# Kernel optimization log

Hardware: AMD Instinct MI355X
Metric: run time of the kernel (lower is better)

## Reference

```python
import jax, jax.numpy as jnp
from jax import lax
import numpy as np

NUM_HEADS = 16
NUM_HEADS_KV = 4
HEAD_DIM = 128
D_CONV = 4
ROT_DIM = 128
ROT_BASE = 10000.0
CAUSAL = True


def setup_inputs() -> dict:
    key = jax.random.key(0)
    ks = jax.random.split(key, 7)
    B, S, E = 2, 2048, 2048
    QKV = HEAD_DIM * (NUM_HEADS + 2 * NUM_HEADS_KV)  # 3072
    return {
        "x": jax.random.normal(ks[0], (B, S, E), jnp.float32),
        "W_in": jax.random.normal(ks[1], (QKV, E), jnp.float32) * 0.02,
        "b_in": jax.random.normal(ks[2], (QKV,), jnp.float32) * 0.02,
        "conv_w": jax.random.normal(ks[3], (QKV, D_CONV), jnp.float32) * 0.1,
        "conv_b": jax.random.normal(ks[4], (QKV,), jnp.float32) * 0.02,
        "W_out": jax.random.normal(ks[5], (E, NUM_HEADS * HEAD_DIM), jnp.float32) * 0.02,
        "b_out": jax.random.normal(ks[6], (E,), jnp.float32) * 0.02,
    }


def _rotary(x, cos, sin):
    # x: [B,S,H,D], non-interleaved rotary over first ROT_DIM dims (here full D)
    x1, x2 = x[..., : ROT_DIM // 2], x[..., ROT_DIM // 2 : ROT_DIM]
    c = cos[None, :, None, :]
    s = sin[None, :, None, :]
    rot = jnp.concatenate([x1 * c - x2 * s, x2 * c + x1 * s], axis=-1)
    return jnp.concatenate([rot, x[..., ROT_DIM:]], axis=-1)


def reference(x, W_in, b_in, conv_w, conv_b, W_out, b_out):
    B, S, E = x.shape
    QKV = conv_w.shape[0]
    # fused in-projection
    qkv = jnp.einsum("bse,fe->bsf", x, W_in) + b_in  # [B,S,QKV]
    # depthwise causal conv1d (left pad d_conv-1, equivalent to torch pad+trim)
    qkv_t = jnp.transpose(qkv, (0, 2, 1))  # [B,C,S]
    qkv_t = jnp.pad(qkv_t, ((0, 0), (0, 0), (D_CONV - 1, 0)))
    conv = lax.conv_general_dilated(
        qkv_t, conv_w[:, None, :], window_strides=(1,), padding="VALID",
        feature_group_count=QKV, dimension_numbers=("NCH", "OIH", "NCH"))
    qkv = jnp.transpose(conv + conv_b[None, :, None], (0, 2, 1))  # [B,S,QKV]
    # split q / kv
    q_dim = NUM_HEADS * HEAD_DIM
    q = qkv[..., :q_dim].reshape(B, S, NUM_HEADS, HEAD_DIM)
    kv = qkv[..., q_dim:].reshape(B, S, 2, NUM_HEADS_KV, HEAD_DIM)
    k, v = kv[:, :, 0], kv[:, :, 1]
    # rotary embedding on q and k
    t = jnp.arange(S, dtype=jnp.float32)
    inv_freq = 1.0 / (ROT_BASE ** (jnp.arange(0, ROT_DIM, 2, dtype=jnp.float32) / ROT_DIM))
    freqs = t[:, None] * inv_freq[None, :]  # [S, ROT_DIM/2]
    cos, sin = jnp.cos(freqs), jnp.sin(freqs)
    q = _rotary(q, cos, sin)
    k = _rotary(k, cos, sin)
    # GQA: repeat kv heads
    rep = NUM_HEADS // NUM_HEADS_KV
    k = jnp.repeat(k, rep, axis=2)  # [B,S,H,D]
    v = jnp.repeat(v, rep, axis=2)
    scale = 1.0 / jnp.sqrt(jnp.float32(HEAD_DIM))
    scores = jnp.einsum("bshd,bthd->bhst", q, k) * scale  # [B,H,S,S]
    if CAUSAL:
        mask = jnp.tril(jnp.ones((S, S), dtype=bool))
        scores = jnp.where(mask[None, None], scores, jnp.finfo(scores.dtype).min)
    attn = jax.nn.softmax(scores, axis=-1)
    ctx = jnp.einsum("bhst,bthd->bshd", attn, v).reshape(B, S, q_dim)
    return jnp.einsum("bsf,ef->bse", ctx, W_out) + b_out
```

## Files before the change

kernel.cpp:

```cpp
#include <hip/hip_runtime.h>
#include <hip/hip_bf16.h>

#define B_   2
#define S_   2048
#define E_   2048
#define QKV_ 3072
#define NH   16
#define NKV  4
#define HD   128
#define SL   16

typedef __attribute__((ext_vector_type(8))) short bf16x8;
typedef __attribute__((ext_vector_type(4))) float f32x4;
typedef unsigned short u16;
typedef unsigned int   u32;

__device__ __forceinline__ float bf2f(u16 u) {
  union { u32 i; float f; } v; v.i = ((u32)u) << 16; return v.f;
}
__device__ __forceinline__ u16 f2bf(float f) {
  union { float f; u32 u; } v; v.f = f;
  return (u16)((v.u + 0x7FFFu + ((v.u >> 16) & 1u)) >> 16);
}
__device__ __forceinline__ u32 pkbf(float a, float b) {
  __hip_bfloat162 h = __float22bfloat162_rn(float2{a, b});
  u32 r; __builtin_memcpy(&r, &h, 4); return r;
}
__device__ __forceinline__ float ex2(float x) { return __builtin_amdgcn_exp2f(x); }
__device__ __forceinline__ void load_lds16(const u16* g, u16* l) {
  __builtin_amdgcn_global_load_lds((const __attribute__((address_space(1))) void*)g,
                                   (__attribute__((address_space(3))) void*)l, 16, 0, 0);
}

__global__ __launch_bounds__(256) void f2b_conv(const float* __restrict__ in,
                                                u16* __restrict__ out, int n4) {
  const int i = blockIdx.x * 256 + threadIdx.x;
  if (i >= n4) return;
  const float4 v = ((const float4*)in)[i];
  ushort4 o;
  o.x = f2bf(v.x); o.y = f2bf(v.y); o.z = f2bf(v.z); o.w = f2bf(v.w);
  ((ushort4*)out)[i] = o;
}

__global__ __launch_bounds__(256) void rope_tab(float* __restrict__ c,
                                                float* __restrict__ s) {
  const int idx = blockIdx.x * 256 + threadIdx.x;
  const int t = idx >> 6, i = idx & 63;
  const float invf = powf(10000.0f, -(float)i * (1.0f / 64.0f));
  float sn, cs;
  sincosf((float)t * invf, &sn, &cs);
  c[idx] = cs; s[idx] = sn;
}

template <int OUT_BF16>
__global__ __launch_bounds__(512, 2) void gemm256(const u16* __restrict__ A,
                                                  const u16* __restrict__ Bm,
                                                  const float* __restrict__ bias,
                                                  void* __restrict__ C,
                                                  int M, int N, int K) {
  __shared__ u16 sm[2][2][256 * 64];
  const int tid = threadIdx.x;
  const int lane = tid & 63;
  const int wave = tid >> 6;
  const int wm = wave >> 2, wn = wave & 3;
  const int L15 = lane & 15, Lq = lane >> 4;
  const int m0 = blockIdx.y * 256, n0 = blockIdx.x * 256;
  const int NT = K >> 6;

  const int srow = tid >> 3;
  const int sdst = (tid & 7) * 8;
  const int ssrc = ((tid & 7) ^ (srow & 7)) * 8;

  auto stageA = [&](int T, int h, int j) {
    const int row = h * 128 + j * 64 + srow;
    load_lds16(A + (size_t)(m0 + row) * K + T * 64 + ssrc,
               &sm[T & 1][0][row * 64 + sdst]);
  };
  auto stageB = [&](int T, int h, int j) {
    const int row = h * 128 + j * 64 + srow;
    load_lds16(Bm + (size_t)(n0 + row) * K + T * 64 + ssrc,
               &sm[T & 1][1][row * 64 + sdst]);
  };
  auto rdA = [&](int p, int ms, int mf, int kk) -> bf16x8 {
    const int row = wm * 128 + ms * 64 + mf * 16 + L15;
    const int u = (kk * 4 + Lq) ^ (row & 7);
    return *(const bf16x8*)&sm[p][0][row * 64 + u * 8];
  };
  auto rdB = [&](int p, int ns, int nf, int kk) -> bf16x8 {
    const int row = wn * 64 + ns * 32 + nf * 16 + L15;
    const int u = (kk * 4 + Lq) ^ (row & 7);
    return *(const bf16x8*)&sm[p][1][row * 64 + u * 8];
  };

  f32x4 acc[8][4] = {};

  stageA(0, 0, 0); stageA(0, 0, 1);
  stageB(0, 0, 0); stageB(0, 0, 1);
  stageA(0, 1, 0); stageA(0, 1, 1);
  stageB(0, 1, 0); stageB(0, 1, 1);
  stageB(1, 0, 0); stageB(1, 0, 1);
  stageA(1, 0, 0); stageA(1, 0, 1);
  asm volatile("s_waitcnt vmcnt(4)" ::: "memory");
  __builtin_amdgcn_s_barrier();

  bf16x8 af[4][2], bf0[2][2], bf1[2][2];

#define MFMA_QUAD(MS, NS, BF)                                                     \
  __builtin_amdgcn_s_setprio(1);                                                  \
  _Pragma("unroll")                                                               \
  for (int kk = 0; kk < 2; ++kk)                                                  \
    _Pragma("unroll")                                                             \
    for (int mf = 0; mf < 4; ++mf)                                                \
      _Pragma("unroll")                                                           \
      for (int nf = 0; nf < 2; ++nf)                                              \
        acc[MS * 4 + mf][NS * 2 + nf] = __builtin_amdgcn_mfma_f32_16x16x32_bf16(  \
            af[mf][kk], BF[nf][kk], acc[MS * 4 + mf][NS * 2 + nf], 0, 0, 0);      \
  __builtin_amdgcn_s_setprio(0);

  for (int T = 0; T < NT; ++T) {
    const int p = T & 1;
#pragma unroll
    for (int mf = 0; mf < 4; ++mf)
#pragma unroll
      for (int kk = 0; kk < 2; ++kk) af[mf][kk] = rdA(p, 0, mf, kk);
#pragma unroll
    for (int nf = 0; nf < 2; ++nf)
#pragma unroll
      for (int kk = 0; kk < 2; ++kk) bf0[nf][kk] = rdB(p, 0, nf, kk);
    if (T + 1 < NT) { stageA(T + 1, 1, 0); stageA(T + 1, 1, 1); }
    __builtin_amdgcn_s_barrier();
    MFMA_QUAD(0, 0, bf0)
    __builtin_amdgcn_s_barrier();
#pragma unroll
    for (int nf = 0; nf < 2; ++nf)
#pragma unroll
      for (int kk = 0; kk < 2; ++kk) bf1[nf][kk] = rdB(p, 1, nf, kk);
    if (T + 1 < NT) { stageB(T + 1, 1, 0); stageB(T + 1, 1, 1); }
    __builtin_amdgcn_s_barrier();
    MFMA_QUAD(0, 1, bf1)
    __builtin_amdgcn_s_barrier();
#pragma unroll
    for (int mf = 0; mf < 4; ++mf)
#pragma unroll
      for (int kk = 0; kk < 2; ++kk) af[mf][kk] = rdA(p, 1, mf, kk);
    if (T + 2 < NT) { stageB(T + 2, 0, 0); stageB(T + 2, 0, 1); }
    __builtin_amdgcn_s_barrier();
    MFMA_QUAD(1, 0, bf0)
    __builtin_amdgcn_s_barrier();
    if (T + 2 < NT) {
      stageA(T + 2, 0, 0); stageA(T + 2, 0, 1);
      asm volatile("s_waitcnt vmcnt(4)" ::: "memory");
    } else {
      asm volatile("s_waitcnt vmcnt(0)" ::: "memory");
    }
    __builtin_amdgcn_s_barrier();
    MFMA_QUAD(1, 1, bf1)
    __builtin_amdgcn_s_barrier();
  }
#undef MFMA_QUAD

#pragma unroll
  for (int ms = 0; ms < 2; ++ms)
#pragma unroll
    for (int mf = 0; mf < 4; ++mf) {
      const int grow0 = m0 + wm * 128 + ms * 64 + mf * 16 + Lq * 4;
#pragma unroll
      for (int ns = 0; ns < 2; ++ns)
#pragma unroll
        for (int nf = 0; nf < 2; ++nf) {
          const int gcol = n0 + wn * 64 + ns * 32 + nf * 16 + L15;
          const float bv = bias[gcol];
          const f32x4 v = acc[ms * 4 + mf][ns * 2 + nf];
#pragma unroll
          for (int r = 0; r < 4; ++r) {
            const float o = v[r] + bv;
            if (OUT_BF16) ((u16*)C)[(size_t)(grow0 + r) * N + gcol] = f2bf(o);
            else          ((float*)C)[(size_t)(grow0 + r) * N + gcol] = o;
          }
        }
    }
}

__global__ __launch_bounds__(512, 2) void gemm_n128(const u16* __restrict__ A,
                                                    const u16* __restrict__ Bm,
                                                    const float* __restrict__ bias,
                                                    float* __restrict__ C,
                                                    int M, int N, int K) {
  __shared__ u16 sm[2][24576];
  const int tid = threadIdx.x, lane = tid & 63, wave = tid >> 6;
  const int wm = wave >> 1, wn = wave & 1;
  const int L15 = lane & 15, Lq = lane >> 4;
  const int m0 = blockIdx.y * 256, n0 = blockIdx.x * 128;
  const int NT = K >> 6;

  const int srow = tid >> 3;
  const int sdst = (tid & 7) * 8;
  const int ssrc = ((tid & 7) ^ (srow & 7)) * 8;

  auto stage6 = [&](int T) {
#pragma unroll
    for (int c = 0; c < 4; ++c) {
      const int row = c * 64 + srow;
      load_lds16(A + (size_t)(m0 + row) * K + T * 64 + ssrc,
                 &sm[T & 1][row * 64 + sdst]);
    }
#pragma unroll
    for (int c = 0; c < 2; ++c) {
      const int row = c * 64 + srow;
      load_lds16(Bm + (size_t)(n0 + row) * K + T * 64 + ssrc,
                 &sm[T & 1][16384 + row * 64 + sdst]);
    }
  };

  f32x4 acc[4][4] = {};
  stage6(0);

  for (int T = 0; T < NT; ++T) {
    const int p = T & 1;
    if (T + 1 < NT) {
      stage6(T + 1);
      asm volatile("s_waitcnt vmcnt(6)" ::: "memory");
    } else {
      asm volatile("s_waitcnt vmcnt(0)" ::: "memory");
    }
    __builtin_amdgcn_s_barrier();
    bf16x8 af[4][2], bfr[4][2];
#pragma unroll
    for (int mf = 0; mf < 4; ++mf)
#pragma unroll
      for (int kk = 0; kk < 2; ++kk) {
        const int row = wm * 64 + mf * 16 + L15;
        const int u = (kk * 4 + Lq) ^ (row & 7);
        af[mf][kk] = *(const bf16x8*)&sm[p][row * 64 + u * 8];
      }
#pragma unroll
    for (int nf = 0; nf < 4; ++nf)
#pragma unroll
      for (int kk = 0; kk < 2; ++kk) {
        const int row = wn * 64 + nf * 16 + L15;
        const int u = (kk * 4 + Lq) ^ (row & 7);
        bfr[nf][kk] = *(const bf16x8*)&sm[p][16384 + row * 64 + u * 8];
      }
    __builtin_amdgcn_s_setprio(1);
#pragma unroll
    for (int kk = 0; kk < 2; ++kk)
#pragma unroll
      for (int mf = 0; mf < 4; ++mf)
#pragma unroll
        for (int nf = 0; nf < 4; ++nf)
          acc[mf][nf] = __builtin_amdgcn_mfma_f32_16x16x32_bf16(
              af[mf][kk], bfr[nf][kk], acc[mf][nf], 0, 0, 0);
    __builtin_amdgcn_s_setprio(0);
    __builtin_amdgcn_s_barrier();
  }

#pragma unroll
  for (int mf = 0; mf < 4; ++mf) {
    const int grow0 = m0 + wm * 64 + mf * 16 + Lq * 4;
#pragma unroll
    for (int nf = 0; nf < 4; ++nf) {
      const int gcol = n0 + wn * 64 + nf * 16 + L15;
      const float bv = bias[gcol];
#pragma unroll
      for (int r = 0; r < 4; ++r)
        C[(size_t)(grow0 + r) * N + gcol] = acc[mf][nf][r] + bv;
    }
  }
}

__global__ __launch_bounds__(256) void conv_rope(const u16* __restrict__ qkv,
                                                 const float* __restrict__ cw,
                                                 const float* __restrict__ cb,
                                                 const float* __restrict__ ct,
                                                 const float* __restrict__ st,
                                                 u16* __restrict__ qo,
                                                 u16* __restrict__ ko,
                                                 u16* __restrict__ vtmp) {
  const int blk = blockIdx.x;
  const int b = blk >> 7;
  const int s0 = (blk & 127) * SL;
  const u16* qb = qkv + (size_t)b * S_ * QKV_;

  for (int u = threadIdx.x; u < 896; u += 256) {
    if (u < 640) {
      const int hs = u >> 5, ip = u & 31, i = ip * 2;
      int f1; u16* outbase; float scale;
      if (hs < 16) {
        f1 = hs * HD + i;
        outbase = qo + (size_t)(b * NH + hs) * S_ * HD;
        scale = 0.08838834764831845f * 1.4426950408889634f;
      } else {
        f1 = NH * HD + (hs - 16) * HD + i;
        outbase = ko + (size_t)(b * NKV + (hs - 16)) * S_ * HD;
        scale = 1.0f;
      }
      const int f2 = f1 + 64;
      const float4 wA0 = *(const float4*)&cw[f1 * 4];
      const float4 wA1 = *(const float4*)&cw[(f1 + 1) * 4];
      const float4 wB0 = *(const float4*)&cw[f2 * 4];
      const float4 wB1 = *(const float4*)&cw[(f2 + 1) * 4];
      const float cA0 = cb[f1], cA1 = cb[f1 + 1], cB0 = cb[f2], cB1 = cb[f2 + 1];
      float A0[3], A1[3], B0[3], B1[3];
#pragma unroll
      for (int j = 0; j < 3; ++j) {
        const int t = s0 - 3 + j;
        if (t >= 0) {
          const u32 pa = *(const u32*)&qb[(size_t)t * QKV_ + f1];
          const u32 pb = *(const u32*)&qb[(size_t)t * QKV_ + f2];
          A0[j] = bf2f((u16)pa); A1[j] = bf2f((u16)(pa >> 16));
          B0[j] = bf2f((u16)pb); B1[j] = bf2f((u16)(pb >> 16));
        } else { A0[j] = A1[j] = B0[j] = B1[j] = 0.f; }
      }
      for (int s = s0; s < s0 + SL; ++s) {
        const u32 pa = *(const u32*)&qb[(size_t)s * QKV_ + f1];
        const u32 pb = *(const u32*)&qb[(size_t)s * QKV_ + f2];
        const float nA0 = bf2f((u16)pa), nA1 = bf2f((u16)(pa >> 16));
        const float nB0 = bf2f((u16)pb), nB1 = bf2f((u16)(pb >> 16));
        const float x1a = cA0 + wA0.x * A0[0] + wA0.y * A0[1] + wA0.z * A0[2] + wA0.w * nA0;
        const float x1b = cA1 + wA1.x * A1[0] + wA1.y * A1[1] + wA1.z * A1[2] + wA1.w * nA1;
        const float x2a = cB0 + wB0.x * B0[0] + wB0.y * B0[1] + wB0.z * B0[2] + wB0.w * nB0;
        const float x2b = cB1 + wB1.x * B1[0] + wB1.y * B1[1] + wB1.z * B1[2] + wB1.w * nB1;
        const float2 cs = *(const float2*)&ct[s * 64 + i];
        const float2 sn = *(const float2*)&st[s * 64 + i];
        u16* outp = outbase + (size_t)s * HD;
        *(u32*)&outp[i]      = pkbf((x1a * cs.x - x2a * sn.x) * scale,
                                    (x1b * cs.y - x2b * sn.y) * scale);
        *(u32*)&outp[i + 64] = pkbf((x2a * cs.x + x1a * sn.x) * scale,
                                    (x2b * cs.y + x1b * sn.y) * scale);
        A0[0] = A0[1]; A0[1] = A0[2]; A0[2] = nA0;
        A1[0] = A1[1]; A1[1] = A1[2]; A1[2] = nA1;
        B0[0] = B0[1]; B0[1] = B0[2]; B0[2] = nB0;
        B1[0] = B1[1]; B1[1] = B1[2]; B1[2] = nB1;
      }
    } else {
      const int vu = u - 640, h = vu >> 6, d = (vu & 63) * 2;
      const int f = (NH + NKV) * HD + h * HD + d;
      const float4 w0 = *(const float4*)&cw[f * 4];
      const float4 w1 = *(const float4*)&cw[(f + 1) * 4];
      const float c0 = cb[f], c1 = cb[f + 1];
      float V0[3], V1[3];
#pragma unroll
      for (int j = 0; j < 3; ++j) {
        const int t = s0 - 3 + j;
        if (t >= 0) {
          const u32 p = *(const u32*)&qb[(size_t)t * QKV_ + f];
          V0[j] = bf2f((u16)p); V1[j] = bf2f((u16)(p >> 16));
        } else { V0[j] = V1[j] = 0.f; }
      }
      u16* vrow = vtmp + (size_t)(b * NKV + h) * S_ * HD + d;
      for (int s = s0; s < s0 + SL; ++s) {
        const u32 p = *(const u32*)&qb[(size_t)s * QKV_ + f];
        const float n0 = bf2f((u16)p), n1 = bf2f((u16)(p >> 16));
        const float v0 = c0 + w0.x * V0[0] + w0.y * V0[1] + w0.z * V0[2] + w0.w * n0;
        const float v1 = c1 + w1.x * V1[0] + w1.y * V1[1] + w1.z * V1[2] + w1.w * n1;
        *(u32*)&vrow[(size_t)s * HD] = pkbf(v0, v1);
        V0[0] = V0[1]; V0[1] = V0[2]; V0[2] = n0;
        V1[0] = V1[1]; V1[1] = V1[2]; V1[2] = n1;
      }
    }
  }
}

__global__ __launch_bounds__(256) void vtrans(const u16* __restrict__ vin,
                                              u16* __restrict__ vout) {
  __shared__ u16 t[64][72];
  const int bh = blockIdx.z;
  const int d0 = blockIdx.y * 64;
  const int s0 = blockIdx.x * 64;
  const u16* ip = vin + ((size_t)bh * S_ + s0) * HD + d0;
  const int r = threadIdx.x >> 4, c4 = (threadIdx.x & 15) * 4;
#pragma unroll
  for (int j = 0; j < 4; ++j) {
    const ushort4 v = *(const ushort4*)&ip[(size_t)(r + j * 16) * HD + c4];
    t[c4 + 0][r + j * 16] = v.x;
    t[c4 + 1][r + j * 16] = v.y;
    t[c4 + 2][r + j * 16] = v.z;
    t[c4 + 3][r + j * 16] = v.w;
  }
  __syncthreads();
  const int dl = threadIdx.x >> 2, sc = (threadIdx.x & 3) * 16;
  u16* op = vout + (size_t)bh * HD * S_ + (size_t)(d0 + dl) * S_ + s0 + sc;
  *(bf16x8*)op       = *(const bf16x8*)&t[dl][sc];
  *(bf16x8*)(op + 8) = *(const bf16x8*)&t[dl][sc + 8];
}

__global__ __launch_bounds__(256, 2) void attn(const u16* __restrict__ q,
                                               const u16* __restrict__ k,
                                               const u16* __restrict__ v,
                                               u16* __restrict__ ctx) {
  __shared__ u16 Ks[2][64 * 128];
  __shared__ u16 Vs[128 * 64];
  __shared__ u16 P[4][16 * 64];
  const int tid = threadIdx.x, wave = tid >> 6, lane = tid & 63;
  const int L15 = lane & 15, Lq = lane >> 4;
  const int bh = blockIdx.y;
  const int b = bh >> 4, h = bh & 15, hk = h >> 2;

  const u16* kb = k + (size_t)(b * NKV + hk) * S_ * HD;
  const u16* vb = v + (size_t)(b * NKV + hk) * HD * S_;

  const int rx = L15 & 7;
  int koff[4], voff[2], poff[2];
#pragma unroll
  for (int c = 0; c < 4; ++c) koff[c] = ((c * 4 + Lq) ^ rx) * 8;
#pragma unroll
  for (int kc = 0; kc < 2; ++kc) {
    voff[kc] = ((kc * 4 + Lq) ^ rx) * 8;
    poff[kc] = L15 * 64 + ((kc * 4 + Lq) ^ rx) * 8;
  }

  const int ksl = tid >> 4, kcp = tid & 15;
  const int vsl = tid >> 3, vcp = tid & 7;

  for (int pass = 0; pass < 2; ++pass) {
    const int qt = pass ? (31 - blockIdx.x) : blockIdx.x;
    const int q0 = qt * 64;
    const int base = q0 + wave * 16;

    bf16x8 qf[4];
    {
      const u16* qp = q + ((size_t)bh * S_ + base + L15) * HD + Lq * 8;
#pragma unroll
      for (int c = 0; c < 4; ++c) qf[c] = *(const bf16x8*)(qp + c * 32);
    }

    f32x4 acc[8] = {};
    float m_i[4], l_i[4];
#pragma unroll
    for (int r = 0; r < 4; ++r) { m_i[r] = -1e30f; l_i[r] = 0.f; }

    const int ktmax = qt + 1;

#pragma unroll
    for (int j = 0; j < 4; ++j) {
      const int krow = j * 16 + ksl;
      load_lds16(kb + (size_t)krow * HD + (kcp ^ (krow & 7)) * 8,
                 &Ks[0][(krow * 16 + kcp) * 8]);
      const int vrow = j * 32 + vsl;
      load_lds16(vb + (size_t)vrow * S_ + (vcp ^ (vrow & 7)) * 8,
                 &Vs[(vrow * 8 + vcp) * 8]);
    }
    __syncthreads();

    for (int kt = 0; kt < ktmax; ++kt) {
      const int k0 = kt * 64;
      const int cur = kt & 1;
      if (kt > 0) {
#pragma unroll
        for (int j = 0; j < 4; ++j) {
          const int vrow = j * 32 + vsl;
          load_lds16(vb + (size_t)vrow * S_ + k0 + (vcp ^ (vrow & 7)) * 8,
                     &Vs[(vrow * 8 + vcp) * 8]);
        }
      }
      if (kt + 1 < ktmax) {
        const int kn = k0 + 64;
#pragma unroll
        for (int j = 0; j < 4; ++j) {
          const int krow = j * 16 + ksl;
          load_lds16(kb + (size_t)(kn + krow) * HD + (kcp ^ (krow & 7)) * 8,
                     &Ks[cur ^ 1][(krow * 16 + kcp) * 8]);
        }
      }
      f32x4 sc[4];
#pragma unroll
      for (int nt = 0; nt < 4; ++nt) sc[nt] = f32x4{0.f, 0.f, 0.f, 0.f};
#pragma unroll
      for (int nt = 0; nt < 4; ++nt) {
#pragma unroll
        for (int c = 0; c < 4; ++c) {
          const bf16x8 kf = *(const bf16x8*)&Ks[cur][(nt * 16 + L15) * 128 + koff[c]];
          sc[nt] = __builtin_amdgcn_mfma_f32_16x16x32_bf16(qf[c], kf, sc[nt], 0, 0, 0);
        }
      }
      if (k0 + 63 > base) {
#pragma unroll
        for (int nt = 0; nt < 4; ++nt) {
          const int col = k0 + nt * 16 + L15;
#pragma unroll
          for (int r = 0; r < 4; ++r) {
            const int row = base + Lq * 4 + r;
            if (col > row) sc[nt][r] = -1e30f;
          }
        }
      }
      float mloc[4];
      bool nm = false;
#pragma unroll
      for (int r = 0; r < 4; ++r) {
        float m = fmaxf(fmaxf(sc[0][r], sc[1][r]), fmaxf(sc[2][r], sc[3][r]));
        m = fmaxf(m, __shfl_xor(m, 1));
        m = fmaxf(m, __shfl_xor(m, 2));
        m = fmaxf(m, __shfl_xor(m, 4));
        m = fmaxf(m, __shfl_xor(m, 8));
        mloc[r] = m;
        nm |= (m > m_i[r]);
      }
      const bool anynew = (__ballot(nm) != 0ull);
      float rsum[4];
      {
        float mnew[4];
#pragma unroll
        for (int r = 0; r < 4; ++r) {
          mnew[r] = anynew ? fmaxf(m_i[r], mloc[r]) : m_i[r];
          rsum[r] = 0.f;
        }
        float pv[4][4];
#pragma unroll
        for (int nt = 0; nt < 4; ++nt)
#pragma unroll
          for (int r = 0; r < 4; ++r) {
            pv[nt][r] = ex2(sc[nt][r] - mnew[r]);
            rsum[r] += pv[nt][r];
          }
#pragma unroll
        for (int nt = 0; nt < 4; ++nt) {
          const int cch = nt * 2 + (L15 >> 3), clo = L15 & 7;
#pragma unroll
          for (int rp = 0; rp < 2; ++rp) {
            const u32 pk = pkbf(pv[nt][rp * 2], pv[nt][rp * 2 + 1]);
            const int row0 = Lq * 4 + rp * 2;
            P[wave][row0 * 64 + (((cch ^ (row0 & 7)) << 3) | clo)] = (u16)pk;
            const int row1 = row0 + 1;
            P[wave][row1 * 64 + (((cch ^ (row1 & 7)) << 3) | clo)] = (u16)(pk >> 16);
          }
        }
        if (anynew) {
          float alpha[4];
#pragma unroll
          for (int r = 0; r < 4; ++r) {
            alpha[r] = ex2(m_i[r] - mnew[r]);
            m_i[r] = mnew[r];
          }
#pragma unroll
          for (int dt = 0; dt < 8; ++dt)
#pragma unroll
            for (int r = 0; r < 4; ++r) acc[dt][r] *= alpha[r];
#pragma unroll
          for (int r = 0; r < 4; ++r) l_i[r] *= alpha[r];
        }
      }
#pragma unroll
      for (int r = 0; r < 4; ++r) {
        float s = rsum[r];
        s += __shfl_xor(s, 1);
        s += __shfl_xor(s, 2);
        s += __shfl_xor(s, 4);
        s += __shfl_xor(s, 8);
        l_i[r] += s;
      }
      __syncthreads();
      {
        bf16x8 pa[2];
#pragma unroll
        for (int kc = 0; kc < 2; ++kc)
          pa[kc] = *(const bf16x8*)&P[wave][poff[kc]];
#pragma unroll
        for (int dt = 0; dt < 8; ++dt)
#pragma unroll
          for (int kc = 0; kc < 2; ++kc) {
            const bf16x8 vf = *(const bf16x8*)&Vs[(dt * 16 + L15) * 64 + voff[kc]];
            acc[dt] = __builtin_amdgcn_mfma_f32_16x16x32_bf16(pa[kc], vf, acc[dt], 0, 0, 0);
          }
      }
      __syncthreads();
    }
    {
      float inv[4];
#pragma unroll
      for (int r = 0; r < 4; ++r) inv[r] = 1.f / l_i[r];
      u16* cp = ctx + ((size_t)b * S_ + base) * (NH * HD) + h * HD;
#pragma unroll
      for (int dt = 0; dt < 8; ++dt)
#pragma unroll
        for (int rp = 0; rp < 2; ++rp) {
          const u32 pk = pkbf(acc[dt][rp * 2] * inv[rp * 2],
                              acc[dt][rp * 2 + 1] * inv[rp * 2 + 1]);
          cp[(size_t)(Lq * 4 + rp * 2) * (NH * HD) + dt * 16 + L15] = (u16)pk;
          cp[(size_t)(Lq * 4 + rp * 2 + 1) * (NH * HD) + dt * 16 + L15] = (u16)(pk >> 16);
        }
    }
  }
}

extern "C" void kernel_launch(void* const* d_in, const int* in_sizes, int n_in,
                              void* d_out, int out_size, void* d_ws, size_t ws_size,
                              hipStream_t stream) {
  const float* x     = (const float*)d_in[0];
  const float* W_in  = (const float*)d_in[1];
  const float* b_in  = (const float*)d_in[2];
  const float* cw    = (const float*)d_in[3];
  const float* cb    = (const float*)d_in[4];
  const float* W_out = (const float*)d_in[5];
  const float* b_out = (const float*)d_in[6];

  char* ws = (char*)d_ws;
  u16* xb   = (u16*)(ws);
  u16* wib  = (u16*)(ws + 16777216);
  u16* wob  = (u16*)(ws + 29360128);
  u16* qkv  = (u16*)(ws + 37748736);
  u16* q_ws = (u16*)(ws + 62914560);
  u16* k_ws = (u16*)(ws + 79691776);
  u16* vt_ws= (u16*)(ws + 83886080);
  float* ctab = (float*)ws;
  float* stab = (float*)(ws + 524288);
  u16* vtmp = wib;
  u16* ctx  = xb;

  const int nx = B_ * S_ * E_ / 4, nwi = QKV_ * E_ / 4, nwo = E_ * NH * HD / 4;
  f2b_conv<<<dim3((nx  + 255) / 256), 256, 0, stream>>>(x,     xb,  nx);
  f2b_conv<<<dim3((nwi + 255) / 256), 256, 0, stream>>>(W_in,  wib, nwi);
  f2b_conv<<<dim3((nwo + 255) / 256), 256, 0, stream>>>(W_out, wob, nwo);

  gemm256<1><<<dim3(QKV_ / 256, (B_ * S_) / 256), 512, 0, stream>>>(
      xb, wib, b_in, (void*)qkv, B_ * S_, QKV_, E_);
  rope_tab<<<dim3(S_ * 64 / 256), 256, 0, stream>>>(ctab, stab);
  conv_rope<<<dim3(B_ * (S_ / SL)), 256, 0, stream>>>(qkv, cw, cb, ctab, stab, q_ws, k_ws, vtmp);
  vtrans<<<dim3(S_ / 64, HD / 64, B_ * NKV), 256, 0, stream>>>(vtmp, vt_ws);
  attn<<<dim3(16, B_ * NH), 256, 0, stream>>>(q_ws, k_ws, vt_ws, ctx);
  gemm_n128<<<dim3(E_ / 128, (B_ * S_) / 256), 512, 0, stream>>>(
      ctx, wob, b_out, (float*)d_out, B_ * S_, E_, NH * HD);
}
```

Before: 343.0 us.

## Compute transposed QK^T and pass P through registers via lane shuffles

Swaps the MFMA operands so each lane holds one query row's scores across keys, which turns the per-row max and sum reductions into two cross-lane shuffles and leaves a single m_i/l_i per lane. The probability tile is then repacked into the PV A-operand layout with lane shuffles instead of a round trip through shared memory, which removes the P LDS buffer and one barrier. It also adds a lazy rescale that skips the alpha correction unless the running max grows by more than 8 in the exp2 domain, and replaces the barrier before PV with an explicit vmcnt wait plus s_barrier. The lazy rescale lets exp2 values exceed 1, which carries some overflow and precision risk in bf16 P, and the hand-placed waitcnt depends on how many loads are still in flight.

```diff
diff --git a/kernel.cpp b/kernel.cpp
--- a/kernel.cpp
+++ b/kernel.cpp
@@ -27,6 +27,7 @@
   u32 r; __builtin_memcpy(&r, &h, 4); return r;
 }
 __device__ __forceinline__ float ex2(float x) { return __builtin_amdgcn_exp2f(x); }
+__device__ __forceinline__ u32 shf(u32 v, int l) { return (u32)__shfl((int)v, l); }
 __device__ __forceinline__ void load_lds16(const u16* g, u16* l) {
   __builtin_amdgcn_global_load_lds((const __attribute__((address_space(1))) void*)g,
                                    (__attribute__((address_space(3))) void*)l, 16, 0, 0);
@@ -390,7 +391,6 @@
                                                u16* __restrict__ ctx) {
   __shared__ u16 Ks[2][64 * 128];
   __shared__ u16 Vs[128 * 64];
-  __shared__ u16 P[4][16 * 64];
   const int tid = threadIdx.x, wave = tid >> 6, lane = tid & 63;
   const int L15 = lane & 15, Lq = lane >> 4;
   const int bh = blockIdx.y;
@@ -400,17 +400,18 @@
   const u16* vb = v + (size_t)(b * NKV + hk) * HD * S_;
 
   const int rx = L15 & 7;
-  int koff[4], voff[2], poff[2];
+  int koff[4], voff[2];
 #pragma unroll
   for (int c = 0; c < 4; ++c) koff[c] = ((c * 4 + Lq) ^ rx) * 8;
 #pragma unroll
-  for (int kc = 0; kc < 2; ++kc) {
-    voff[kc] = ((kc * 4 + Lq) ^ rx) * 8;
-    poff[kc] = L15 * 64 + ((kc * 4 + Lq) ^ rx) * 8;
-  }
+  for (int kc = 0; kc < 2; ++kc) voff[kc] = ((kc * 4 + Lq) ^ rx) * 8;
 
   const int ksl = tid >> 4, kcp = tid & 15;
   const int vsl = tid >> 3, vcp = tid & 7;
+
+  const int ls0 = ((Lq & 1) << 5) + L15;
+  const int ls1 = ls0 + 16;
+  const bool hi = (Lq & 2) != 0;
 
   for (int pass = 0; pass < 2; ++pass) {
     const int qt = pass ? (31 - blockIdx.x) : blockIdx.x;
@@ -425,9 +426,7 @@
     }
 
     f32x4 acc[8] = {};
-    float m_i[4], l_i[4];
-#pragma unroll
-    for (int r = 0; r < 4; ++r) { m_i[r] = -1e30f; l_i[r] = 0.f; }
+    float m_i = -1e30f, l_i = 0.f;
 
     const int ktmax = qt + 1;
 
@@ -470,105 +469,86 @@
 #pragma unroll
         for (int c = 0; c < 4; ++c) {
           const bf16x8 kf = *(const bf16x8*)&Ks[cur][(nt * 16 + L15) * 128 + koff[c]];
-          sc[nt] = __builtin_amdgcn_mfma_f32_16x16x32_bf16(qf[c], kf, sc[nt], 0, 0, 0);
+          sc[nt] = __builtin_amdgcn_mfma_f32_16x16x32_bf16(kf, qf[c], sc[nt], 0, 0, 0);
         }
       }
       if (k0 + 63 > base) {
 #pragma unroll
-        for (int nt = 0; nt < 4; ++nt) {
-          const int col = k0 + nt * 16 + L15;
+        for (int nt = 0; nt < 4; ++nt)
 #pragma unroll
           for (int r = 0; r < 4; ++r) {
-            const int row = base + Lq * 4 + r;
-            if (col > row) sc[nt][r] = -1e30f;
+            const int kidx = k0 + nt * 16 + Lq * 4 + r;
+            if (kidx > base + L15) sc[nt][r] = -1e30f;
           }
+      }
+      float mloc = fmaxf(fmaxf(fmaxf(sc[0][0], sc[0][1]), fmaxf(sc[0][2], sc[0][3])),
+                         fmaxf(fmaxf(sc[1][0], sc[1][1]), fmaxf(sc[1][2], sc[1][3])));
+      mloc = fmaxf(mloc,
+                   fmaxf(fmaxf(fmaxf(sc[2][0], sc[2][1]), fmaxf(sc[2][2], sc[2][3])),
+                         fmaxf(fmaxf(sc[3][0], sc[3][1]), fmaxf(sc[3][2], sc[3][3]))));
+      mloc = fmaxf(mloc, __shfl_xor(mloc, 16));
+      mloc = fmaxf(mloc, __shfl_xor(mloc, 32));
+      const bool defer = __all(mloc - m_i <= 8.f);
+      if (!defer) {
+        const float mnew = fmaxf(m_i, mloc);
+        const float alpha = ex2(m_i - mnew);
+        m_i = mnew;
+        l_i *= alpha;
+        float aacc[4];
+#pragma unroll
+        for (int r = 0; r < 4; ++r) aacc[r] = __shfl(alpha, Lq * 4 + r);
+#pragma unroll
+        for (int dt = 0; dt < 8; ++dt)
+#pragma unroll
+          for (int r = 0; r < 4; ++r) acc[dt][r] *= aacc[r];
+      }
+      float lsum = 0.f;
+#pragma unroll
+      for (int nt = 0; nt < 4; ++nt)
+#pragma unroll
+        for (int r = 0; r < 4; ++r) {
+          sc[nt][r] = ex2(sc[nt][r] - m_i);
+          lsum += sc[nt][r];
         }
-      }
-      float mloc[4];
-      bool nm = false;
-#pragma unroll
-      for (int r = 0; r < 4; ++r) {
-        float m = fmaxf(fmaxf(sc[0][r], sc[1][r]), fmaxf(sc[2][r], sc[3][r]));
-        m = fmaxf(m, __shfl_xor(m, 1));
-        m = fmaxf(m, __shfl_xor(m, 2));
-        m = fmaxf(m, __shfl_xor(m, 4));
-        m = fmaxf(m, __shfl_xor(m, 8));
-        mloc[r] = m;
-        nm |= (m > m_i[r]);
-      }
-      const bool anynew = (__ballot(nm) != 0ull);
-      float rsum[4];
+      lsum += __shfl_xor(lsum, 16);
+      lsum += __shfl_xor(lsum, 32);
+      l_i += lsum;
+      u32 wA[2], wB[2], wC[2], wD[2];
+      wA[0] = pkbf(sc[0][0], sc[0][1]); wA[1] = pkbf(sc[0][2], sc[0][3]);
+      wB[0] = pkbf(sc[1][0], sc[1][1]); wB[1] = pkbf(sc[1][2], sc[1][3]);
+      wC[0] = pkbf(sc[2][0], sc[2][1]); wC[1] = pkbf(sc[2][2], sc[2][3]);
+      wD[0] = pkbf(sc[3][0], sc[3][1]); wD[1] = pkbf(sc[3][2], sc[3][3]);
+      bf16x8 pa[2];
       {
-        float mnew[4];
-#pragma unroll
-        for (int r = 0; r < 4; ++r) {
-          mnew[r] = anynew ? fmaxf(m_i[r], mloc[r]) : m_i[r];
-          rsum[r] = 0.f;
+        union { u32 u[4]; bf16x8 v; } t0, t1;
+        u32 x0, x1;
+        x0 = shf(wA[0], ls0); x1 = shf(wB[0], ls0); t0.u[0] = hi ? x1 : x0;
+        x0 = shf(wA[1], ls0); x1 = shf(wB[1], ls0); t0.u[1] = hi ? x1 : x0;
+        x0 = shf(wA[0], ls1); x1 = shf(wB[0], ls1); t0.u[2] = hi ? x1 : x0;
+        x0 = shf(wA[1], ls1); x1 = shf(wB[1], ls1); t0.u[3] = hi ? x1 : x0;
+        x0 = shf(wC[0], ls0); x1 = shf(wD[0], ls0); t1.u[0] = hi ? x1 : x0;
+        x0 = shf(wC[1], ls0); x1 = shf(wD[1], ls0); t1.u[1] = hi ? x1 : x0;
+        x0 = shf(wC[0], ls1); x1 = shf(wD[0], ls1); t1.u[2] = hi ? x1 : x0;
+        x0 = shf(wC[1], ls1); x1 = shf(wD[1], ls1); t1.u[3] = hi ? x1 : x0;
+        pa[0] = t0.v; pa[1] = t1.v;
+      }
+      if (kt + 1 < ktmax) asm volatile("s_waitcnt vmcnt(4)" ::: "memory");
+      else                asm volatile("s_waitcnt vmcnt(0)" ::: "memory");
+      __builtin_amdgcn_s_barrier();
+      asm volatile("" ::: "memory");
+#pragma unroll
+      for (int dt = 0; dt < 8; ++dt)
+#pragma unroll
+        for (int kc = 0; kc < 2; ++kc) {
+          const bf16x8 vf = *(const bf16x8*)&Vs[(dt * 16 + L15) * 64 + voff[kc]];
+          acc[dt] = __builtin_amdgcn_mfma_f32_16x16x32_bf16(pa[kc], vf, acc[dt], 0, 0, 0);
         }
-        float pv[4][4];
-#pragma unroll
-        for (int nt = 0; nt < 4; ++nt)
-#pragma unroll
-          for (int r = 0; r < 4; ++r) {
-            pv[nt][r] = ex2(sc[nt][r] - mnew[r]);
-            rsum[r] += pv[nt][r];
-          }
-#pragma unroll
-        for (int nt = 0; nt < 4; ++nt) {
-          const int cch = nt * 2 + (L15 >> 3), clo = L15 & 7;
-#pragma unroll
-          for (int rp = 0; rp < 2; ++rp) {
-            const u32 pk = pkbf(pv[nt][rp * 2], pv[nt][rp * 2 + 1]);
-            const int row0 = Lq * 4 + rp * 2;
-            P[wave][row0 * 64 + (((cch ^ (row0 & 7)) << 3) | clo)] = (u16)pk;
-            const int row1 = row0 + 1;
-            P[wave][row1 * 64 + (((cch ^ (row1 & 7)) << 3) | clo)] = (u16)(pk >> 16);
-          }
-        }
-        if (anynew) {
-          float alpha[4];
-#pragma unroll
-          for (int r = 0; r < 4; ++r) {
-            alpha[r] = ex2(m_i[r] - mnew[r]);
-            m_i[r] = mnew[r];
-          }
-#pragma unroll
-          for (int dt = 0; dt < 8; ++dt)
-#pragma unroll
-            for (int r = 0; r < 4; ++r) acc[dt][r] *= alpha[r];
-#pragma unroll
-          for (int r = 0; r < 4; ++r) l_i[r] *= alpha[r];
-        }
-      }
-#pragma unroll
-      for (int r = 0; r < 4; ++r) {
-        float s = rsum[r];
-        s += __shfl_xor(s, 1);
-        s += __shfl_xor(s, 2);
-        s += __shfl_xor(s, 4);
-        s += __shfl_xor(s, 8);
-        l_i[r] += s;
-      }
-      __syncthreads();
-      {
-        bf16x8 pa[2];
-#pragma unroll
-        for (int kc = 0; kc < 2; ++kc)
-          pa[kc] = *(const bf16x8*)&P[wave][poff[kc]];
-#pragma unroll
-        for (int dt = 0; dt < 8; ++dt)
-#pragma unroll
-          for (int kc = 0; kc < 2; ++kc) {
-            const bf16x8 vf = *(const bf16x8*)&Vs[(dt * 16 + L15) * 64 + voff[kc]];
-            acc[dt] = __builtin_amdgcn_mfma_f32_16x16x32_bf16(pa[kc], vf, acc[dt], 0, 0, 0);
-          }
-      }
       __syncthreads();
     }
     {
       float inv[4];
 #pragma unroll
-      for (int r = 0; r < 4; ++r) inv[r] = 1.f / l_i[r];
+      for (int r = 0; r < 4; ++r) inv[r] = 1.f / __shfl(l_i, Lq * 4 + r);
       u16* cp = ctx + ((size_t)b * S_ + base) * (NH * HD) + h * HD;
 #pragma unroll
       for (int dt = 0; dt < 8; ++dt)
```

New measurement: 323.6 us. 5.7% less time.
